# Optimization experiments

Hardware: AMD Instinct MI355X
Metric: run time of the kernel (lower is better)

## Reference

```python
import jax, jax.numpy as jnp
import numpy as np

B, T, N, C, H = 64, 12, 1370, 8, 64

def setup_inputs() -> dict:
    key = jax.random.key(0)
    ks = jax.random.split(key, 7)
    s_ih = 1.0 / np.sqrt(H)
    inp = {
        "x": jax.random.normal(ks[0], (B, T, N, C), dtype=jnp.float32),
        # PyTorch nn.LSTM params, gate order (i, f, g, o)
        "W_ih": jax.random.uniform(ks[1], (4 * H, C), jnp.float32, -s_ih, s_ih),
        "W_hh": jax.random.uniform(ks[2], (4 * H, H), jnp.float32, -s_ih, s_ih),
        "b_ih": jax.random.uniform(ks[3], (4 * H,), jnp.float32, -s_ih, s_ih),
        "b_hh": jax.random.uniform(ks[4], (4 * H,), jnp.float32, -s_ih, s_ih),
        "W_fc": jax.random.uniform(ks[5], (C, H), jnp.float32, -s_ih, s_ih),
        "b_fc": jax.random.uniform(ks[6], (C,), jnp.float32, -s_ih, s_ih),
    }
    return inp

def reference(x, W_ih, W_hh, b_ih, b_hh, W_fc, b_fc):
    Bx, Tx, Nx, Cx = x.shape
    Hh = W_hh.shape[1]
    # (B, T, N, C) -> (B*N, T, C): shared-weight LSTM over all node sequences
    xr = jnp.transpose(x, (0, 2, 1, 3)).reshape(Bx * Nx, Tx, Cx)
    # Precompute input projections for all timesteps: (B*N, T, 4H)
    x_gates = jnp.einsum('btc,gc->btg', xr, W_ih) + b_ih
    # time-major for scan: (T, B*N, 4H)
    x_gates = jnp.moveaxis(x_gates, 1, 0)

    def step(carry, xg):
        h, c = carry
        gates = xg + h @ W_hh.T + b_hh  # (B*N, 4H)
        i, f, g, o = jnp.split(gates, 4, axis=-1)
        i = jax.nn.sigmoid(i)
        f = jax.nn.sigmoid(f)
        g = jnp.tanh(g)
        o = jax.nn.sigmoid(o)
        c = f * c + i * g
        h = o * jnp.tanh(c)
        return (h, c), None

    h0 = jnp.zeros((Bx * Nx, Hh), dtype=x.dtype)
    c0 = jnp.zeros((Bx * Nx, Hh), dtype=x.dtype)
    (h_last, _), _ = jax.lax.scan(step, (h0, c0), x_gates)

    y_flat = h_last @ W_fc.T + b_fc  # (B*N, C)
    return y_flat.reshape(Bx, Nx, Cx)
```

## Files before the change

### kernel.cpp

```cpp
#include <hip/hip_runtime.h>

#define T_ 12
#define N_ 1370
#define C_ 8
#define H_ 64
#define MSEQ 32
#define NT 2
#define LDA 88
#define NBLK 2740

typedef __attribute__((ext_vector_type(8))) short short8;
typedef __attribute__((ext_vector_type(4))) float floatx4;

#define NLOG2E -1.4426950408889634f
#define TLOG2E 2.8853901817779268f

__device__ __forceinline__ short f2bf(float x) {
  unsigned u = __builtin_bit_cast(unsigned, x);
  u = (u + 0x7fffu + ((u >> 16) & 1u)) >> 16;
  return (short)u;
}
__device__ __forceinline__ unsigned pk_bf16(float a, float b) {
  unsigned r;
  asm("v_cvt_pk_bf16_f32 %0, %1, %2" : "=v"(r) : "v"(a), "v"(b));
  return r;
}
__device__ __forceinline__ short8 load_w8s(const float* __restrict__ p, float s) {
  short8 r;
#pragma unroll
  for (int j = 0; j < 8; ++j) r[j] = f2bf(p[j] * s);
  return r;
}

__global__ void __launch_bounds__(256) lstm_kernel(
    const float* __restrict__ x, const float* __restrict__ W_ih,
    const float* __restrict__ W_hh, const float* __restrict__ b_ih,
    const float* __restrict__ b_hh, const float* __restrict__ W_fc,
    const float* __restrict__ b_fc, float* __restrict__ out) {
  __shared__ short A[2][MSEQ][LDA];

  const int tid = threadIdx.x;
  const int wave = tid >> 6;
  const int lane = tid & 63;
  const int m16 = lane & 15;
  const int q = lane >> 4;
  const int blk = blockIdx.x;

  const int u = wave * 16 + m16;
  short8 bf[4][3];
  float bias[4];
#pragma unroll
  for (int g = 0; g < 4; ++g) {
    const float sg = (g == 2) ? TLOG2E : NLOG2E;
    const int grow = g * 64 + u;
    const float* wr = W_hh + grow * 64;
    bf[g][0] = load_w8s(wr + q * 8, sg);
    bf[g][1] = load_w8s(wr + 32 + q * 8, sg);
    if (q == 0) {
      bf[g][2] = load_w8s(W_ih + grow * 8, sg);
    } else {
      short8 z = {0, 0, 0, 0, 0, 0, 0, 0};
      bf[g][2] = z;
    }
    bias[g] = sg * (b_ih[grow] + b_hh[grow]);
  }

  const int xrow = tid >> 3;
  const int xcol = tid & 7;
  const int s0 = blk * MSEQ + xrow;
  const int bidx = s0 / N_;
  const int nidx = s0 - bidx * N_;
  const float* xptr = x + ((size_t)bidx * T_ * N_ + nidx) * C_ + xcol;

  {
    int* Ai = (int*)A;
#pragma unroll
    for (int i = 0; i < (2 * MSEQ * LDA) / (2 * 256); ++i)
      Ai[i * 256 + tid] = 0;
  }
  __syncthreads();
  A[0][xrow][64 + xcol] = f2bf(*xptr);
  __syncthreads();

  float cst[NT][4];
#pragma unroll
  for (int mt = 0; mt < NT; ++mt)
#pragma unroll
    for (int r = 0; r < 4; ++r) cst[mt][r] = 0.0f;

  for (int t = 0; t < T_; ++t) {
    const int rb = t & 1, wb = rb ^ 1;
#pragma unroll
    for (int mt = 0; mt < NT; ++mt) {
      const short* arow = &A[rb][mt * 16 + m16][0];
      short8 a0 = *(const short8*)(arow + q * 8);
      short8 a1 = *(const short8*)(arow + 32 + q * 8);
      short8 a2 = *(const short8*)(arow + 64 + q * 8);
      floatx4 gi = {bias[0], bias[0], bias[0], bias[0]};
      floatx4 gf = {bias[1], bias[1], bias[1], bias[1]};
      floatx4 gg = {bias[2], bias[2], bias[2], bias[2]};
      floatx4 go = {bias[3], bias[3], bias[3], bias[3]};
      gi = __builtin_amdgcn_mfma_f32_16x16x32_bf16(a0, bf[0][0], gi, 0, 0, 0);
      gf = __builtin_amdgcn_mfma_f32_16x16x32_bf16(a0, bf[1][0], gf, 0, 0, 0);
      gg = __builtin_amdgcn_mfma_f32_16x16x32_bf16(a0, bf[2][0], gg, 0, 0, 0);
      go = __builtin_amdgcn_mfma_f32_16x16x32_bf16(a0, bf[3][0], go, 0, 0, 0);
      gi = __builtin_amdgcn_mfma_f32_16x16x32_bf16(a1, bf[0][1], gi, 0, 0, 0);
      gf = __builtin_amdgcn_mfma_f32_16x16x32_bf16(a1, bf[1][1], gf, 0, 0, 0);
      gg = __builtin_amdgcn_mfma_f32_16x16x32_bf16(a1, bf[2][1], gg, 0, 0, 0);
      go = __builtin_amdgcn_mfma_f32_16x16x32_bf16(a1, bf[3][1], go, 0, 0, 0);
      gi = __builtin_amdgcn_mfma_f32_16x16x32_bf16(a2, bf[0][2], gi, 0, 0, 0);
      gf = __builtin_amdgcn_mfma_f32_16x16x32_bf16(a2, bf[1][2], gf, 0, 0, 0);
      gg = __builtin_amdgcn_mfma_f32_16x16x32_bf16(a2, bf[2][2], gg, 0, 0, 0);
      go = __builtin_amdgcn_mfma_f32_16x16x32_bf16(a2, bf[3][2], go, 0, 0, 0);
      float hv[4];
#pragma unroll
      for (int r = 0; r < 4; ++r) {
        float iv = __builtin_amdgcn_rcpf(1.0f + __builtin_amdgcn_exp2f(gi[r]));
        float fv = __builtin_amdgcn_rcpf(1.0f + __builtin_amdgcn_exp2f(gf[r]));
        float gv = fmaf(-2.0f, __builtin_amdgcn_rcpf(1.0f + __builtin_amdgcn_exp2f(gg[r])), 1.0f);
        float ov = __builtin_amdgcn_rcpf(1.0f + __builtin_amdgcn_exp2f(go[r]));
        float cc = fmaf(fv, cst[mt][r], iv * gv);
        cst[mt][r] = cc;
        float tc = fmaf(-2.0f, __builtin_amdgcn_rcpf(1.0f + __builtin_amdgcn_exp2f(cc * TLOG2E)), 1.0f);
        hv[r] = ov * tc;
      }
      unsigned p01 = pk_bf16(hv[0], hv[1]);
      unsigned p23 = pk_bf16(hv[2], hv[3]);
      const int rbase = mt * 16 + q * 4;
      A[wb][rbase + 0][u] = (short)p01;
      A[wb][rbase + 1][u] = (short)(p01 >> 16);
      A[wb][rbase + 2][u] = (short)p23;
      A[wb][rbase + 3][u] = (short)(p23 >> 16);
    }
    if (t + 1 < T_) {
      A[wb][xrow][64 + xcol] = f2bf(xptr[(size_t)(t + 1) * (N_ * C_)]);
    }
    __syncthreads();
  }

  if (wave < NT) {
    short8 fb0, fb1;
    float fbias = 0.0f;
    if (m16 < 8) {
      const float* wr = W_fc + m16 * 64;
      fb0 = load_w8s(wr + q * 8, 1.0f);
      fb1 = load_w8s(wr + 32 + q * 8, 1.0f);
      fbias = b_fc[m16];
    } else {
      short8 z = {0, 0, 0, 0, 0, 0, 0, 0};
      fb0 = z;
      fb1 = z;
    }
    const int mt = wave;
    const short* arow = &A[0][mt * 16 + m16][0];
    short8 a0 = *(const short8*)(arow + q * 8);
    short8 a1 = *(const short8*)(arow + 32 + q * 8);
    floatx4 acc = {fbias, fbias, fbias, fbias};
    acc = __builtin_amdgcn_mfma_f32_16x16x32_bf16(a0, fb0, acc, 0, 0, 0);
    acc = __builtin_amdgcn_mfma_f32_16x16x32_bf16(a1, fb1, acc, 0, 0, 0);
    if (m16 < 8) {
      const int srow = blk * MSEQ + mt * 16 + q * 4;
#pragma unroll
      for (int r = 0; r < 4; ++r) out[(srow + r) * 8 + m16] = acc[r];
    }
  }
}

extern "C" void kernel_launch(void* const* d_in, const int* in_sizes, int n_in,
                              void* d_out, int out_size, void* d_ws,
                              size_t ws_size, hipStream_t stream) {
  const float* x    = (const float*)d_in[0];
  const float* W_ih = (const float*)d_in[1];
  const float* W_hh = (const float*)d_in[2];
  const float* b_ih = (const float*)d_in[3];
  const float* b_hh = (const float*)d_in[4];
  const float* W_fc = (const float*)d_in[5];
  const float* b_fc = (const float*)d_in[6];
  float* out = (float*)d_out;
  hipLaunchKernelGGL(lstm_kernel, dim3(NBLK), dim3(256), 0, stream,
                     x, W_ih, W_hh, b_ih, b_hh, W_fc, b_fc, out);
}
```

Measured before the change: 181.3 us.

## Transpose MFMA operands, preload all x timesteps to LDS, fold bias into GEMM

```diff
diff --git a/kernel.cpp b/kernel.cpp
--- a/kernel.cpp
+++ b/kernel.cpp
@@ -2,18 +2,16 @@
 
 #define T_ 12
 #define N_ 1370
-#define C_ 8
-#define H_ 64
 #define MSEQ 32
-#define NT 2
-#define LDA 88
+#define LDA 72
+#define LDX 20
 #define NBLK 2740
 
 typedef __attribute__((ext_vector_type(8))) short short8;
 typedef __attribute__((ext_vector_type(4))) float floatx4;
 
 #define NLOG2E -1.4426950408889634f
-#define TLOG2E 2.8853901817779268f
+#define TLOG2E 2.8853900817779268f
 
 __device__ __forceinline__ short f2bf(float x) {
   unsigned u = __builtin_bit_cast(unsigned, x);
@@ -32,12 +30,13 @@
   return r;
 }
 
-__global__ void __launch_bounds__(256) lstm_kernel(
+__global__ void __launch_bounds__(256, 4) lstm_kernel(
     const float* __restrict__ x, const float* __restrict__ W_ih,
     const float* __restrict__ W_hh, const float* __restrict__ b_ih,
     const float* __restrict__ b_hh, const float* __restrict__ W_fc,
     const float* __restrict__ b_fc, float* __restrict__ out) {
-  __shared__ short A[2][MSEQ][LDA];
+  __shared__ short hbuf[2][MSEQ][LDA];
+  __shared__ short xls[T_][MSEQ][LDX];
 
   const int tid = threadIdx.x;
   const int wave = tid >> 6;
@@ -46,122 +45,127 @@
   const int q = lane >> 4;
   const int blk = blockIdx.x;
 
-  const int u = wave * 16 + m16;
-  short8 bf[4][3];
-  float bias[4];
+  const int urow = wave * 16 + m16;
+  short8 wA[4][3];
 #pragma unroll
   for (int g = 0; g < 4; ++g) {
     const float sg = (g == 2) ? TLOG2E : NLOG2E;
-    const int grow = g * 64 + u;
+    const int grow = g * 64 + urow;
     const float* wr = W_hh + grow * 64;
-    bf[g][0] = load_w8s(wr + q * 8, sg);
-    bf[g][1] = load_w8s(wr + 32 + q * 8, sg);
+    wA[g][0] = load_w8s(wr + q * 8, sg);
+    wA[g][1] = load_w8s(wr + 32 + q * 8, sg);
+    short8 z = {0, 0, 0, 0, 0, 0, 0, 0};
     if (q == 0) {
-      bf[g][2] = load_w8s(W_ih + grow * 8, sg);
+      wA[g][2] = load_w8s(W_ih + grow * 8, sg);
+    } else if (q == 1) {
+      z[0] = f2bf(sg * (b_ih[grow] + b_hh[grow]));
+      wA[g][2] = z;
     } else {
-      short8 z = {0, 0, 0, 0, 0, 0, 0, 0};
-      bf[g][2] = z;
+      wA[g][2] = z;
     }
-    bias[g] = sg * (b_ih[grow] + b_hh[grow]);
   }
 
-  const int xrow = tid >> 3;
-  const int xcol = tid & 7;
-  const int s0 = blk * MSEQ + xrow;
-  const int bidx = s0 / N_;
-  const int nidx = s0 - bidx * N_;
-  const float* xptr = x + ((size_t)bidx * T_ * N_ + nidx) * C_ + xcol;
+  {
+    int* hp = (int*)hbuf;
+#pragma unroll
+    for (int i = tid; i < (2 * MSEQ * LDA) / 2; i += 256) hp[i] = 0;
+    int* xp = (int*)xls;
+#pragma unroll
+    for (int i = tid; i < (T_ * MSEQ * LDX) / 2; i += 256) xp[i] = 0;
+  }
+  __syncthreads();
 
   {
-    int* Ai = (int*)A;
+    const int xseq = tid >> 3, xc = tid & 7;
+    const int s0 = blk * MSEQ + xseq;
+    const int bidx = s0 / N_;
+    const int nidx = s0 - bidx * N_;
+    const float* xp = x + ((size_t)(bidx * T_) * N_ + nidx) * 8 + xc;
 #pragma unroll
-    for (int i = 0; i < (2 * MSEQ * LDA) / (2 * 256); ++i)
-      Ai[i * 256 + tid] = 0;
+    for (int t = 0; t < T_; ++t) {
+      xls[t][xseq][xc] = f2bf(xp[(size_t)t * (N_ * 8)]);
+      if (xc == 0) xls[t][xseq][8] = (short)0x3F80;
+    }
   }
   __syncthreads();
-  A[0][xrow][64 + xcol] = f2bf(*xptr);
-  __syncthreads();
 
-  float cst[NT][4];
+  const int xoff = q ? 8 : 0;
+  const floatx4 zacc = {0.0f, 0.0f, 0.0f, 0.0f};
+
+  float cst[2][4];
 #pragma unroll
-  for (int mt = 0; mt < NT; ++mt)
+  for (int nt = 0; nt < 2; ++nt)
 #pragma unroll
-    for (int r = 0; r < 4; ++r) cst[mt][r] = 0.0f;
+    for (int r = 0; r < 4; ++r) cst[nt][r] = 0.0f;
 
   for (int t = 0; t < T_; ++t) {
     const int rb = t & 1, wb = rb ^ 1;
 #pragma unroll
-    for (int mt = 0; mt < NT; ++mt) {
-      const short* arow = &A[rb][mt * 16 + m16][0];
-      short8 a0 = *(const short8*)(arow + q * 8);
-      short8 a1 = *(const short8*)(arow + 32 + q * 8);
-      short8 a2 = *(const short8*)(arow + 64 + q * 8);
-      floatx4 gi = {bias[0], bias[0], bias[0], bias[0]};
-      floatx4 gf = {bias[1], bias[1], bias[1], bias[1]};
-      floatx4 gg = {bias[2], bias[2], bias[2], bias[2]};
-      floatx4 go = {bias[3], bias[3], bias[3], bias[3]};
-      gi = __builtin_amdgcn_mfma_f32_16x16x32_bf16(a0, bf[0][0], gi, 0, 0, 0);
-      gf = __builtin_amdgcn_mfma_f32_16x16x32_bf16(a0, bf[1][0], gf, 0, 0, 0);
-      gg = __builtin_amdgcn_mfma_f32_16x16x32_bf16(a0, bf[2][0], gg, 0, 0, 0);
-      go = __builtin_amdgcn_mfma_f32_16x16x32_bf16(a0, bf[3][0], go, 0, 0, 0);
-      gi = __builtin_amdgcn_mfma_f32_16x16x32_bf16(a1, bf[0][1], gi, 0, 0, 0);
-      gf = __builtin_amdgcn_mfma_f32_16x16x32_bf16(a1, bf[1][1], gf, 0, 0, 0);
-      gg = __builtin_amdgcn_mfma_f32_16x16x32_bf16(a1, bf[2][1], gg, 0, 0, 0);
-      go = __builtin_amdgcn_mfma_f32_16x16x32_bf16(a1, bf[3][1], go, 0, 0, 0);
-      gi = __builtin_amdgcn_mfma_f32_16x16x32_bf16(a2, bf[0][2], gi, 0, 0, 0);
-      gf = __builtin_amdgcn_mfma_f32_16x16x32_bf16(a2, bf[1][2], gf, 0, 0, 0);
-      gg = __builtin_amdgcn_mfma_f32_16x16x32_bf16(a2, bf[2][2], gg, 0, 0, 0);
-      go = __builtin_amdgcn_mfma_f32_16x16x32_bf16(a2, bf[3][2], go, 0, 0, 0);
+    for (int nt = 0; nt < 2; ++nt) {
+      const int srow = nt * 16 + m16;
+      short8 b0 = *(const short8*)&hbuf[rb][srow][q * 8];
+      short8 b1 = *(const short8*)&hbuf[rb][srow][32 + q * 8];
+      short8 bx = *(const short8*)&xls[t][srow][xoff];
+      floatx4 gi = __builtin_amdgcn_mfma_f32_16x16x32_bf16(wA[0][0], b0, zacc, 0, 0, 0);
+      floatx4 gf = __builtin_amdgcn_mfma_f32_16x16x32_bf16(wA[1][0], b0, zacc, 0, 0, 0);
+      floatx4 gg = __builtin_amdgcn_mfma_f32_16x16x32_bf16(wA[2][0], b0, zacc, 0, 0, 0);
+      floatx4 go = __builtin_amdgcn_mfma_f32_16x16x32_bf16(wA[3][0], b0, zacc, 0, 0, 0);
+      gi = __builtin_amdgcn_mfma_f32_16x16x32_bf16(wA[0][1], b1, gi, 0, 0, 0);
+      gf = __builtin_amdgcn_mfma_f32_16x16x32_bf16(wA[1][1], b1, gf, 0, 0, 0);
+      gg = __builtin_amdgcn_mfma_f32_16x16x32_bf16(wA[2][1], b1, gg, 0, 0, 0);
+      go = __builtin_amdgcn_mfma_f32_16x16x32_bf16(wA[3][1], b1, go, 0, 0, 0);
+      gi = __builtin_amdgcn_mfma_f32_16x16x32_bf16(wA[0][2], bx, gi, 0, 0, 0);
+      gf = __builtin_amdgcn_mfma_f32_16x16x32_bf16(wA[1][2], bx, gf, 0, 0, 0);
+      gg = __builtin_amdgcn_mfma_f32_16x16x32_bf16(wA[2][2], bx, gg, 0, 0, 0);
+      go = __builtin_amdgcn_mfma_f32_16x16x32_bf16(wA[3][2], bx, go, 0, 0, 0);
       float hv[4];
 #pragma unroll
       for (int r = 0; r < 4; ++r) {
-        float iv = __builtin_amdgcn_rcpf(1.0f + __builtin_amdgcn_exp2f(gi[r]));
-        float fv = __builtin_amdgcn_rcpf(1.0f + __builtin_amdgcn_exp2f(gf[r]));
-        float gv = fmaf(-2.0f, __builtin_amdgcn_rcpf(1.0f + __builtin_amdgcn_exp2f(gg[r])), 1.0f);
-        float ov = __builtin_amdgcn_rcpf(1.0f + __builtin_amdgcn_exp2f(go[r]));
-        float cc = fmaf(fv, cst[mt][r], iv * gv);
-        cst[mt][r] = cc;
-        float tc = fmaf(-2.0f, __builtin_amdgcn_rcpf(1.0f + __builtin_amdgcn_exp2f(cc * TLOG2E)), 1.0f);
+        float di = 1.0f + __builtin_amdgcn_exp2f(gi[r]);
+        float df = 1.0f + __builtin_amdgcn_exp2f(gf[r]);
+        float dg = 1.0f + __builtin_amdgcn_exp2f(gg[r]);
+        float dq = 1.0f + __builtin_amdgcn_exp2f(go[r]);
+        float pa = di * df, pb = dg * dq;
+        float rp = __builtin_amdgcn_rcpf(pa * pb);
+        float iv = rp * df * pb;
+        float fv = rp * di * pb;
+        float gv = fmaf(-2.0f, rp * pa * dq, 1.0f);
+        float ov = rp * pa * dg;
+        float cc = fmaf(fv, cst[nt][r], iv * gv);
+        cst[nt][r] = cc;
+        float dt = 1.0f + __builtin_amdgcn_exp2f(cc * TLOG2E);
+        float tc = fmaf(-2.0f, __builtin_amdgcn_rcpf(dt), 1.0f);
         hv[r] = ov * tc;
       }
-      unsigned p01 = pk_bf16(hv[0], hv[1]);
-      unsigned p23 = pk_bf16(hv[2], hv[3]);
-      const int rbase = mt * 16 + q * 4;
-      A[wb][rbase + 0][u] = (short)p01;
-      A[wb][rbase + 1][u] = (short)(p01 >> 16);
-      A[wb][rbase + 2][u] = (short)p23;
-      A[wb][rbase + 3][u] = (short)(p23 >> 16);
-    }
-    if (t + 1 < T_) {
-      A[wb][xrow][64 + xcol] = f2bf(xptr[(size_t)(t + 1) * (N_ * C_)]);
+      unsigned long long pk =
+          (unsigned long long)pk_bf16(hv[0], hv[1]) |
+          ((unsigned long long)pk_bf16(hv[2], hv[3]) << 32);
+      *(unsigned long long*)&hbuf[wb][srow][wave * 16 + q * 4] = pk;
     }
     __syncthreads();
   }
 
-  if (wave < NT) {
-    short8 fb0, fb1;
-    float fbias = 0.0f;
+  if (wave < 2) {
+    short8 f0, f1;
+    short8 z = {0, 0, 0, 0, 0, 0, 0, 0};
     if (m16 < 8) {
       const float* wr = W_fc + m16 * 64;
-      fb0 = load_w8s(wr + q * 8, 1.0f);
-      fb1 = load_w8s(wr + 32 + q * 8, 1.0f);
-      fbias = b_fc[m16];
+      f0 = load_w8s(wr + q * 8, 1.0f);
+      f1 = load_w8s(wr + 32 + q * 8, 1.0f);
     } else {
-      short8 z = {0, 0, 0, 0, 0, 0, 0, 0};
-      fb0 = z;
-      fb1 = z;
+      f0 = z;
+      f1 = z;
     }
-    const int mt = wave;
-    const short* arow = &A[0][mt * 16 + m16][0];
-    short8 a0 = *(const short8*)(arow + q * 8);
-    short8 a1 = *(const short8*)(arow + 32 + q * 8);
-    floatx4 acc = {fbias, fbias, fbias, fbias};
-    acc = __builtin_amdgcn_mfma_f32_16x16x32_bf16(a0, fb0, acc, 0, 0, 0);
-    acc = __builtin_amdgcn_mfma_f32_16x16x32_bf16(a1, fb1, acc, 0, 0, 0);
-    if (m16 < 8) {
-      const int srow = blk * MSEQ + mt * 16 + q * 4;
+    const int srow = wave * 16 + m16;
+    short8 h0 = *(const short8*)&hbuf[0][srow][q * 8];
+    short8 h1 = *(const short8*)&hbuf[0][srow][32 + q * 8];
+    floatx4 acc = __builtin_amdgcn_mfma_f32_16x16x32_bf16(f0, h0, zacc, 0, 0, 0);
+    acc = __builtin_amdgcn_mfma_f32_16x16x32_bf16(f1, h1, acc, 0, 0, 0);
+    if (q < 2) {
+      const int orow = blk * MSEQ + srow;
 #pragma unroll
-      for (int r = 0; r < 4; ++r) out[(srow + r) * 8 + m16] = acc[r];
+      for (int r = 0; r < 4; ++r)
+        out[orow * 8 + q * 4 + r] = acc[r] + b_fc[q * 4 + r];
     }
   }
 }
```

Result: faster. 169.9 us (-6.3%).
